# Optimization experiments

Hardware: AMD Instinct MI355X
Metric: run time of the kernel (lower is better)

The kernel has to match this reference:

```python
import jax, jax.numpy as jnp
import numpy as np

D_MODEL = 1024
N_HEAD = 16
N_KV_HEAD = 4
D_K = D_MODEL // N_HEAD          # 64
N_REP = N_HEAD // N_KV_HEAD      # 4
B, S = 2, 2048


def setup_inputs() -> dict:
    key = jax.random.key(0)
    ks = jax.random.split(key, 7)
    scale = 1.0 / np.sqrt(D_MODEL)
    return {
        "q": jax.random.normal(ks[0], (B, S, D_MODEL), jnp.float32),
        "k": jax.random.normal(ks[1], (B, S, D_MODEL), jnp.float32),
        "v": jax.random.normal(ks[2], (B, S, D_MODEL), jnp.float32),
        # weights stored [in, out] (nn.Linear applies x @ W.T; we fold the transpose)
        "W_q": jax.random.normal(ks[3], (D_MODEL, N_HEAD * D_K), jnp.float32) * scale,
        "W_k": jax.random.normal(ks[4], (D_MODEL, N_KV_HEAD * D_K), jnp.float32) * scale,
        "W_v": jax.random.normal(ks[5], (D_MODEL, N_KV_HEAD * D_K), jnp.float32) * scale,
        "W_o": jax.random.normal(ks[6], (D_MODEL, D_MODEL), jnp.float32) * scale,
    }


def reference(q, k, v, W_q, W_k, W_v, W_o):
    batch, seq_q, _ = q.shape
    seq_k = k.shape[1]
    # projections -> [b, h, s, d]
    Q = (q @ W_q).reshape(batch, seq_q, N_HEAD, D_K).transpose(0, 2, 1, 3)
    K = (k @ W_k).reshape(batch, seq_k, N_KV_HEAD, D_K).transpose(0, 2, 1, 3)
    V = (v @ W_v).reshape(batch, seq_k, N_KV_HEAD, D_K).transpose(0, 2, 1, 3)
    # repeat each KV head n_rep times consecutively (matches expand+reshape)
    K = jnp.repeat(K, N_REP, axis=1)  # [b, n_head, seq_k, d_k]
    V = jnp.repeat(V, N_REP, axis=1)
    scores = jnp.einsum('bhqd,bhkd->bhqk', Q, K) / np.sqrt(D_K).astype(jnp.float32)
    attn = jax.nn.softmax(scores, axis=-1)
    out = jnp.einsum('bhqk,bhkd->bhqd', attn, V)  # [b, h, seq_q, d_k]
    out = out.transpose(0, 2, 1, 3).reshape(batch, seq_q, D_MODEL)
    return out @ W_o
```

## Files before the change

### kernel.cpp

```cpp
#include <hip/hip_runtime.h>
#include <hip/hip_bf16.h>
#include <stdint.h>

#define DEVINL __device__ __forceinline__

typedef unsigned short u16;
typedef __bf16 bf16x8 __attribute__((ext_vector_type(8)));
typedef float f32x4 __attribute__((ext_vector_type(4)));
typedef float f32x16 __attribute__((ext_vector_type(16)));
typedef unsigned short u16x8 __attribute__((ext_vector_type(8)));
typedef unsigned int u32x4 __attribute__((ext_vector_type(4)));

constexpr int BATCH = 2, SEQ = 2048, DM = 1024, NH = 16, NKVH = 4, DK = 64;
#define QSCALE 0.18033688f

DEVINL u16 f2bf(float f) {
    unsigned u = __builtin_bit_cast(unsigned, f);
    u += 0x7fffu + ((u >> 16) & 1u);
    return (u16)(u >> 16);
}

DEVINL unsigned pkbf(float a, float b) {
    unsigned r;
    asm("v_cvt_pk_bf16_f32 %0, %1, %2" : "=v"(r) : "v"(a), "v"(b));
    return r;
}
DEVINL void swap32(unsigned& a, unsigned& b) {
    asm("v_permlane32_swap_b32 %0, %1" : "+v"(a), "+v"(b));
}
DEVINL float fexp2(float x) {
    float r;
    asm("v_exp_f32 %0, %1" : "=v"(r) : "v"(x));
    return r;
}

DEVINL void gload16(const void* g, void* l) {
    __builtin_amdgcn_global_load_lds(
        (const __attribute__((address_space(1))) unsigned int*)g,
        (__attribute__((address_space(3))) unsigned int*)l, 16, 0, 0);
}

DEVINL bf16x8 ldfrag(const u16* p) { return *reinterpret_cast<const bf16x8*>(p); }

__global__ __launch_bounds__(256) void prep_kernel(
    const float* __restrict__ q, const float* __restrict__ k, const float* __restrict__ v,
    const float* __restrict__ Wq, const float* __restrict__ Wk,
    const float* __restrict__ Wv, const float* __restrict__ Wo,
    u16* __restrict__ qb, u16* __restrict__ kb, u16* __restrict__ vb,
    u16* __restrict__ Wqt, u16* __restrict__ Wkt,
    u16* __restrict__ Wvt, u16* __restrict__ Wot) {
    __shared__ float tile[32][33];
    int bid = blockIdx.x;
    if (bid < 6144) {
        const float* in;
        u16* out;
        switch (bid >> 11) {
            case 0: in = q; out = qb; break;
            case 1: in = k; out = kb; break;
            default: in = v; out = vb; break;
        }
        int i = (bid & 2047) * 256 + threadIdx.x;
        const float4* p = reinterpret_cast<const float4*>(in) + (size_t)i * 2;
        float4 a = p[0], b = p[1];
        u16x8 o;
        o[0] = f2bf(a.x); o[1] = f2bf(a.y); o[2] = f2bf(a.z); o[3] = f2bf(a.w);
        o[4] = f2bf(b.x); o[5] = f2bf(b.y); o[6] = f2bf(b.z); o[7] = f2bf(b.w);
        reinterpret_cast<u16x8*>(out)[i] = o;
    } else {
        int tb = bid - 6144;
        int z = tb >> 10, rem = tb & 1023;
        const float* W;
        u16* Wt;
        int N;
        switch (z) {
            case 0: W = Wq; Wt = Wqt; N = 1024; break;
            case 1: W = Wk; Wt = Wkt; N = 256; break;
            case 2: W = Wv; Wt = Wvt; N = 256; break;
            default: W = Wo; Wt = Wot; N = 1024; break;
        }
        int n0 = (rem & 31) * 32;
        if (n0 >= N) return;
        int k0 = (rem >> 5) * 32;
        int tx = threadIdx.x & 31, ty = threadIdx.x >> 5;
#pragma unroll
        for (int r = 0; r < 4; ++r)
            tile[ty + 8 * r][tx] = W[(size_t)(k0 + ty + 8 * r) * N + n0 + tx];
        __syncthreads();
#pragma unroll
        for (int r = 0; r < 4; ++r)
            Wt[(size_t)(n0 + ty + 8 * r) * 1024 + k0 + tx] = f2bf(tile[tx][ty + 8 * r]);
    }
}

#define GEMM_CORE64(Apt, Bpt)                                                 \
    __shared__ __align__(16) u16 Al[2][128 * 32];                             \
    __shared__ __align__(16) u16 Bl[2][64 * 32];                              \
    const int tid = threadIdx.x;                                              \
    const int lane = tid & 63;                                                \
    const int w = tid >> 6;                                                   \
    const u16* Ab = (Apt) + (size_t)m0 * 1024;                                \
    const u16* Bb = (Bpt) + (size_t)n0 * 1024;                                \
    f32x4 acc[2][4] = {};                                                     \
    auto stage = [&](int buf, int kt) {                                       \
        const u16* Ag = Ab + kt * 32;                                         \
        const u16* Bg = Bb + kt * 32;                                         \
        _Pragma("unroll") for (int rnd = 0; rnd < 2; ++rnd) {                 \
            int L = tid * 16 + rnd * 4096;                                    \
            int row = L >> 6;                                                 \
            int cb = (L & 63) ^ (((row >> 1) & 3) << 4);                      \
            gload16(Ag + (size_t)row * 1024 + (cb >> 1), &Al[buf][L >> 1]);   \
        }                                                                     \
        {                                                                     \
            int L = tid * 16;                                                 \
            int row = L >> 6;                                                 \
            int cb = (L & 63) ^ (((row >> 1) & 3) << 4);                      \
            gload16(Bg + (size_t)row * 1024 + (cb >> 1), &Bl[buf][L >> 1]);   \
        }                                                                     \
    };                                                                        \
    stage(0, 0);                                                              \
    __syncthreads();                                                          \
    int buf = 0;                                                              \
    for (int kt = 0; kt < 32; ++kt) {                                         \
        if (kt + 1 < 32) stage(buf ^ 1, kt + 1);                              \
        bf16x8 af[2], bfr[4];                                                 \
        _Pragma("unroll") for (int mi = 0; mi < 2; ++mi) {                    \
            int row = w * 32 + mi * 16 + (lane & 15);                         \
            int cb = ((lane >> 4) * 16) ^ (((row >> 1) & 3) << 4);            \
            af[mi] = ldfrag(&Al[buf][row * 32 + (cb >> 1)]);                  \
        }                                                                     \
        _Pragma("unroll") for (int ni = 0; ni < 4; ++ni) {                    \
            int row = ni * 16 + (lane & 15);                                  \
            int cb = ((lane >> 4) * 16) ^ (((row >> 1) & 3) << 4);            \
            bfr[ni] = ldfrag(&Bl[buf][row * 32 + (cb >> 1)]);                 \
        }                                                                     \
        _Pragma("unroll") for (int mi = 0; mi < 2; ++mi)                      \
            _Pragma("unroll") for (int ni = 0; ni < 4; ++ni)                  \
                acc[mi][ni] = __builtin_amdgcn_mfma_f32_16x16x32_bf16(        \
                    af[mi], bfr[ni], acc[mi][ni], 0, 0, 0);                   \
        __syncthreads();                                                      \
        buf ^= 1;                                                             \
    }

__global__ __launch_bounds__(256) void proj_kernel(
    const u16* __restrict__ qb, const u16* __restrict__ kb, const u16* __restrict__ vb,
    const u16* __restrict__ Wqt, const u16* __restrict__ Wkt, const u16* __restrict__ Wvt,
    u16* __restrict__ Qp, u16* __restrict__ Kf, u16* __restrict__ Vf) {
    int bid = blockIdx.x;
    int tile = (bid & 7) * 96 + (bid >> 3);
    const u16 *A, *Bt;
    int m0, n0, z;
    if (tile < 512) {
        z = 0; A = qb; Bt = Wqt; m0 = (tile >> 4) * 128; n0 = (tile & 15) * 64;
    } else if (tile < 640) {
        int t = tile - 512;
        z = 1; A = kb; Bt = Wkt; m0 = (t >> 2) * 128; n0 = (t & 3) * 64;
    } else {
        int t = tile - 640;
        z = 2; A = vb; Bt = Wvt; m0 = (t >> 2) * 128; n0 = (t & 3) * 64;
    }

    GEMM_CORE64(A, Bt)

#pragma unroll
    for (int mi = 0; mi < 2; ++mi)
#pragma unroll
        for (int ni = 0; ni < 4; ++ni)
#pragma unroll
            for (int r = 0; r < 4; ++r) {
                int row = m0 + w * 32 + mi * 16 + (lane >> 4) * 4 + r;
                int col = n0 + ni * 16 + (lane & 15);
                float v = acc[mi][ni][r];
                int bb = row >> 11, s = row & 2047;
                int hh = col >> 6, dd = col & 63;
                if (z == 0) {
                    Qp[((((size_t)bb * NH + hh) * 2048 + s) << 6) + dd] = f2bf(v * QSCALE);
                } else if (z == 1) {
                    size_t base = (size_t)(bb * NKVH + hh) * 131072;
                    int s32 = s >> 5, q31s = s & 31;
                    int c = dd >> 4, hib = (dd >> 3) & 1, j = dd & 7;
                    Kf[base + (size_t)((s32 * 4 + c) * 64 + hib * 32 + q31s) * 8 + j] = f2bf(v);
                } else {
                    size_t base = (size_t)(bb * NKVH + hh) * 131072;
                    int kt = s >> 6, i = (s >> 4) & 3, hib = (s >> 3) & 1, j = s & 7;
                    int dt = dd >> 5, q31v = dd & 31;
                    Vf[base + (size_t)((((kt * 2 + dt) * 4 + i) * 64) + hib * 32 + q31v) * 8 + j] = f2bf(v);
                }
            }
}

__global__ __launch_bounds__(256) void oproj_kernel(const u16* __restrict__ Oa,
                                                    const u16* __restrict__ Wot,
                                                    float* __restrict__ out) {
    int bid = blockIdx.x;
    int tile = (bid & 7) * 64 + (bid >> 3);
    const int m0 = (tile >> 4) * 128, n0 = (tile & 15) * 64;

    GEMM_CORE64(Oa, Wot)

#pragma unroll
    for (int mi = 0; mi < 2; ++mi)
#pragma unroll
        for (int ni = 0; ni < 4; ++ni)
#pragma unroll
            for (int r = 0; r < 4; ++r) {
                int row = m0 + w * 32 + mi * 16 + (lane >> 4) * 4 + r;
                int col = n0 + ni * 16 + (lane & 15);
                out[(size_t)row * 1024 + col] = acc[mi][ni][r];
            }
}

__global__ __launch_bounds__(256) void attn_kernel(const u16* __restrict__ Qp,
                                                   const u16* __restrict__ Kf,
                                                   const u16* __restrict__ Vf,
                                                   u16* __restrict__ Oa) {
    __shared__ __align__(16) u16 Kl[4][4096];
    __shared__ __align__(16) u16 Vl[4][4096];

    const int tid = threadIdx.x;
    const int lane = tid & 63, w = tid >> 6;
    const int hi = lane >> 5, q31 = lane & 31;
    const int qt = blockIdx.x, h = blockIdx.y, b = blockIdx.z;
    const int kvh = h >> 2;
    const int qrow = qt * 128 + w * 32 + q31;

    const u16* Qb = Qp + ((size_t)((b * NH + h) * SEQ) + qrow) * 64 + hi * 8;
    bf16x8 qf0 = ldfrag(Qb), qf1 = ldfrag(Qb + 16);
    bf16x8 qf2 = ldfrag(Qb + 32), qf3 = ldfrag(Qb + 48);

    const u16* KbG = Kf + (size_t)(b * NKVH + kvh) * 131072;
    const u16* VbG = Vf + (size_t)(b * NKVH + kvh) * 131072;

    auto stageT = [&](int slot, int tile) {
        const u16* Kg = KbG + (size_t)tile * 4096 + lane * 8;
        const u16* Vg = VbG + (size_t)tile * 4096 + lane * 8;
        gload16(Kg + w * 512, &Kl[slot][w * 512]);
        gload16(Kg + (w + 4) * 512, &Kl[slot][(w + 4) * 512]);
        gload16(Vg + w * 512, &Vl[slot][w * 512]);
        gload16(Vg + (w + 4) * 512, &Vl[slot][(w + 4) * 512]);
    };

    f32x16 od0 = {}, od1 = {};
    float lsum = 0.f;
    f32x16 sA0 = {}, sA1 = {}, sB0 = {}, sB1 = {};
    bf16x8 kA[8], kB[8], vf[8];

    stageT(0, 0);
    stageT(1, 1);
    stageT(2, 2);
    asm volatile("s_waitcnt vmcnt(0)" ::: "memory");
    __builtin_amdgcn_s_barrier();

#pragma unroll
    for (int r = 0; r < 8; ++r) kA[r] = ldfrag(&Kl[0][r * 512 + lane * 8]);
    sA0 = __builtin_amdgcn_mfma_f32_32x32x16_bf16(kA[0], qf0, sA0, 0, 0, 0);
    sA0 = __builtin_amdgcn_mfma_f32_32x32x16_bf16(kA[1], qf1, sA0, 0, 0, 0);
    sA0 = __builtin_amdgcn_mfma_f32_32x32x16_bf16(kA[2], qf2, sA0, 0, 0, 0);
    sA0 = __builtin_amdgcn_mfma_f32_32x32x16_bf16(kA[3], qf3, sA0, 0, 0, 0);
    sA1 = __builtin_amdgcn_mfma_f32_32x32x16_bf16(kA[4], qf0, sA1, 0, 0, 0);
    sA1 = __builtin_amdgcn_mfma_f32_32x32x16_bf16(kA[5], qf1, sA1, 0, 0, 0);
    sA1 = __builtin_amdgcn_mfma_f32_32x32x16_bf16(kA[6], qf2, sA1, 0, 0, 0);
    sA1 = __builtin_amdgcn_mfma_f32_32x32x16_bf16(kA[7], qf3, sA1, 0, 0, 0);
#pragma unroll
    for (int r = 0; r < 8; ++r) kB[r] = ldfrag(&Kl[1][r * 512 + lane * 8]);
#pragma unroll
    for (int r = 0; r < 8; ++r) vf[r] = ldfrag(&Vl[0][r * 512 + lane * 8]);

#define PACKP(sv, s, outf)                                    \
        {                                                     \
            unsigned x0 = pkbf(sv[8 * s + 0], sv[8 * s + 1]); \
            unsigned x1 = pkbf(sv[8 * s + 2], sv[8 * s + 3]); \
            unsigned y0 = pkbf(sv[8 * s + 4], sv[8 * s + 5]); \
            unsigned y1 = pkbf(sv[8 * s + 6], sv[8 * s + 7]); \
            swap32(x0, y0);                                   \
            swap32(x1, y1);                                   \
            u32x4 tt2 = {x0, x1, y0, y1};                     \
            outf = __builtin_bit_cast(bf16x8, tt2);           \
        }

#define BODY(SC0, SC1, SN0, SN1, KQK, KLD, T)                                 \
    {                                                                         \
        __builtin_amdgcn_s_setprio(1);                                        \
        SN0 = {};                                                             \
        SN1 = {};                                                             \
        SN0 = __builtin_amdgcn_mfma_f32_32x32x16_bf16(KQK[0], qf0, SN0, 0, 0, 0); \
        SN0 = __builtin_amdgcn_mfma_f32_32x32x16_bf16(KQK[1], qf1, SN0, 0, 0, 0); \
        SN0 = __builtin_amdgcn_mfma_f32_32x32x16_bf16(KQK[2], qf2, SN0, 0, 0, 0); \
        SN0 = __builtin_amdgcn_mfma_f32_32x32x16_bf16(KQK[3], qf3, SN0, 0, 0, 0); \
        SN1 = __builtin_amdgcn_mfma_f32_32x32x16_bf16(KQK[4], qf0, SN1, 0, 0, 0); \
        SN1 = __builtin_amdgcn_mfma_f32_32x32x16_bf16(KQK[5], qf1, SN1, 0, 0, 0); \
        SN1 = __builtin_amdgcn_mfma_f32_32x32x16_bf16(KQK[6], qf2, SN1, 0, 0, 0); \
        SN1 = __builtin_amdgcn_mfma_f32_32x32x16_bf16(KQK[7], qf3, SN1, 0, 0, 0); \
        __builtin_amdgcn_s_setprio(0);                                        \
        stageT(((T) + 3) & 3, ((T) + 3) & 31);                                \
        {                                                                     \
            const u16* Ksl = &Kl[((T) + 2) & 3][lane * 8];                    \
            _Pragma("unroll") for (int r = 0; r < 8; ++r)                     \
                KLD[r] = ldfrag(Ksl + r * 512);                               \
        }                                                                     \
        _Pragma("unroll") for (int r = 0; r < 16; ++r) {                      \
            SC0[r] = fexp2(SC0[r]);                                           \
            SC1[r] = fexp2(SC1[r]);                                           \
        }                                                                     \
        {                                                                     \
            f32x16 ts = SC0 + SC1;                                            \
            float u0 = (ts[0] + ts[1]) + (ts[2] + ts[3]);                     \
            float u1 = (ts[4] + ts[5]) + (ts[6] + ts[7]);                     \
            float u2 = (ts[8] + ts[9]) + (ts[10] + ts[11]);                   \
            float u3 = (ts[12] + ts[13]) + (ts[14] + ts[15]);                 \
            lsum += (u0 + u1) + (u2 + u3);                                    \
        }                                                                     \
        bf16x8 pa0, pa1, pa2, pa3;                                            \
        PACKP(SC0, 0, pa0)                                                    \
        PACKP(SC0, 1, pa1)                                                    \
        PACKP(SC1, 0, pa2)                                                    \
        PACKP(SC1, 1, pa3)                                                    \
        __builtin_amdgcn_s_setprio(1);                                        \
        od0 = __builtin_amdgcn_mfma_f32_32x32x16_bf16(vf[0], pa0, od0, 0, 0, 0); \
        od0 = __builtin_amdgcn_mfma_f32_32x32x16_bf16(vf[1], pa1, od0, 0, 0, 0); \
        od0 = __builtin_amdgcn_mfma_f32_32x32x16_bf16(vf[2], pa2, od0, 0, 0, 0); \
        od0 = __builtin_amdgcn_mfma_f32_32x32x16_bf16(vf[3], pa3, od0, 0, 0, 0); \
        od1 = __builtin_amdgcn_mfma_f32_32x32x16_bf16(vf[4], pa0, od1, 0, 0, 0); \
        od1 = __builtin_amdgcn_mfma_f32_32x32x16_bf16(vf[5], pa1, od1, 0, 0, 0); \
        od1 = __builtin_amdgcn_mfma_f32_32x32x16_bf16(vf[6], pa2, od1, 0, 0, 0); \
        od1 = __builtin_amdgcn_mfma_f32_32x32x16_bf16(vf[7], pa3, od1, 0, 0, 0); \
        __builtin_amdgcn_s_setprio(0);                                        \
        {                                                                     \
            const u16* Vsl = &Vl[((T) + 1) & 3][lane * 8];                    \
            _Pragma("unroll") for (int r = 0; r < 8; ++r)                     \
                vf[r] = ldfrag(Vsl + r * 512);                                \
        }                                                                     \
        asm volatile("s_waitcnt vmcnt(0)" ::: "memory");                      \
        __builtin_amdgcn_s_barrier();                                         \
    }

    for (int tt = 0; tt < 16; ++tt) {
        int t = tt * 2;
        BODY(sA0, sA1, sB0, sB1, kB, kA, t)
        BODY(sB0, sB1, sA0, sA1, kA, kB, t + 1)
    }
#undef BODY
#undef PACKP

    lsum += __shfl_xor(lsum, 32);

    float inv = 1.0f / lsum;
    u16* Ob = Oa + ((size_t)(b * SEQ) + qrow) * DM + h * 64;
#pragma unroll
    for (int i = 0; i < 8; ++i) {
        int r = 2 * i;
        int d = (r & 3) + 8 * (r >> 2) + 4 * hi;
        *(unsigned*)(Ob + d) = pkbf(od0[r] * inv, od0[r + 1] * inv);
        *(unsigned*)(Ob + 32 + d) = pkbf(od1[r] * inv, od1[r + 1] * inv);
    }
}

extern "C" void kernel_launch(void* const* d_in, const int* in_sizes, int n_in,
                              void* d_out, int out_size, void* d_ws, size_t ws_size,
                              hipStream_t stream) {
    const float* q  = (const float*)d_in[0];
    const float* k  = (const float*)d_in[1];
    const float* v  = (const float*)d_in[2];
    const float* Wq = (const float*)d_in[3];
    const float* Wk = (const float*)d_in[4];
    const float* Wv = (const float*)d_in[5];
    const float* Wo = (const float*)d_in[6];
    float* out = (float*)d_out;

    char* ws = (char*)d_ws;
    u16* qb  = (u16*)(ws + (size_t)0);
    u16* kb  = (u16*)(ws + ((size_t)8 << 20));
    u16* vb  = (u16*)(ws + ((size_t)16 << 20));
    u16* Wqt = (u16*)(ws + ((size_t)24 << 20));
    u16* Wkt = (u16*)(ws + ((size_t)26 << 20));
    u16* Wvt = (u16*)(ws + ((size_t)27 << 20));
    u16* Wot = (u16*)(ws + ((size_t)28 << 20));
    u16* Qp  = (u16*)(ws + ((size_t)30 << 20));
    u16* Kf  = (u16*)(ws + ((size_t)38 << 20));
    u16* Vf  = (u16*)(ws + ((size_t)40 << 20));
    u16* Oa  = (u16*)(ws + ((size_t)42 << 20));

    prep_kernel<<<10240, 256, 0, stream>>>(q, k, v, Wq, Wk, Wv, Wo,
                                           qb, kb, vb, Wqt, Wkt, Wvt, Wot);

    proj_kernel<<<768, 256, 0, stream>>>(qb, kb, vb, Wqt, Wkt, Wvt,
                                         Qp, Kf, Vf);

    attn_kernel<<<dim3(16, 16, 2), 256, 0, stream>>>(Qp, Kf, Vf, Oa);

    oproj_kernel<<<512, 256, 0, stream>>>(Oa, Wot, out);
}
```

Measured before the change: 113.9 us.

## Fuse fp32-to-bf16 activation conversion into projection GEMM; compute softmax sum via MFMA

The prep kernel no longer converts q/k/v to bf16. The projection kernel now loads fp32 activations straight into registers, packs them to bf16 and writes them into swizzled LDS, prefetching one k-tile ahead. This removes a full read and write of the bf16 activation copies. In attention, the softmax row sum is now accumulated with an MFMA against a ones vector instead of scalar adds and a shuffle, and score accumulators start from a zero constant. The MFMA sum uses the bf16-rounded probabilities, which adds some MFMA work and slightly changes numerics.

```diff
diff --git a/kernel.cpp b/kernel.cpp
--- a/kernel.cpp
+++ b/kernel.cpp
@@ -43,53 +43,33 @@
 DEVINL bf16x8 ldfrag(const u16* p) { return *reinterpret_cast<const bf16x8*>(p); }
 
 __global__ __launch_bounds__(256) void prep_kernel(
-    const float* __restrict__ q, const float* __restrict__ k, const float* __restrict__ v,
     const float* __restrict__ Wq, const float* __restrict__ Wk,
     const float* __restrict__ Wv, const float* __restrict__ Wo,
-    u16* __restrict__ qb, u16* __restrict__ kb, u16* __restrict__ vb,
     u16* __restrict__ Wqt, u16* __restrict__ Wkt,
     u16* __restrict__ Wvt, u16* __restrict__ Wot) {
     __shared__ float tile[32][33];
     int bid = blockIdx.x;
-    if (bid < 6144) {
-        const float* in;
-        u16* out;
-        switch (bid >> 11) {
-            case 0: in = q; out = qb; break;
-            case 1: in = k; out = kb; break;
-            default: in = v; out = vb; break;
-        }
-        int i = (bid & 2047) * 256 + threadIdx.x;
-        const float4* p = reinterpret_cast<const float4*>(in) + (size_t)i * 2;
-        float4 a = p[0], b = p[1];
-        u16x8 o;
-        o[0] = f2bf(a.x); o[1] = f2bf(a.y); o[2] = f2bf(a.z); o[3] = f2bf(a.w);
-        o[4] = f2bf(b.x); o[5] = f2bf(b.y); o[6] = f2bf(b.z); o[7] = f2bf(b.w);
-        reinterpret_cast<u16x8*>(out)[i] = o;
-    } else {
-        int tb = bid - 6144;
-        int z = tb >> 10, rem = tb & 1023;
-        const float* W;
-        u16* Wt;
-        int N;
-        switch (z) {
-            case 0: W = Wq; Wt = Wqt; N = 1024; break;
-            case 1: W = Wk; Wt = Wkt; N = 256; break;
-            case 2: W = Wv; Wt = Wvt; N = 256; break;
-            default: W = Wo; Wt = Wot; N = 1024; break;
-        }
-        int n0 = (rem & 31) * 32;
-        if (n0 >= N) return;
-        int k0 = (rem >> 5) * 32;
-        int tx = threadIdx.x & 31, ty = threadIdx.x >> 5;
-#pragma unroll
-        for (int r = 0; r < 4; ++r)
-            tile[ty + 8 * r][tx] = W[(size_t)(k0 + ty + 8 * r) * N + n0 + tx];
-        __syncthreads();
-#pragma unroll
-        for (int r = 0; r < 4; ++r)
-            Wt[(size_t)(n0 + ty + 8 * r) * 1024 + k0 + tx] = f2bf(tile[tx][ty + 8 * r]);
-    }
+    int z = bid >> 10, rem = bid & 1023;
+    const float* W;
+    u16* Wt;
+    int N;
+    switch (z) {
+        case 0: W = Wq; Wt = Wqt; N = 1024; break;
+        case 1: W = Wk; Wt = Wkt; N = 256; break;
+        case 2: W = Wv; Wt = Wvt; N = 256; break;
+        default: W = Wo; Wt = Wot; N = 1024; break;
+    }
+    int n0 = (rem & 31) * 32;
+    if (n0 >= N) return;
+    int k0 = (rem >> 5) * 32;
+    int tx = threadIdx.x & 31, ty = threadIdx.x >> 5;
+#pragma unroll
+    for (int r = 0; r < 4; ++r)
+        tile[ty + 8 * r][tx] = W[(size_t)(k0 + ty + 8 * r) * N + n0 + tx];
+    __syncthreads();
+#pragma unroll
+    for (int r = 0; r < 4; ++r)
+        Wt[(size_t)(n0 + ty + 8 * r) * 1024 + k0 + tx] = f2bf(tile[tx][ty + 8 * r]);
 }
 
 #define GEMM_CORE64(Apt, Bpt)                                                 \
@@ -142,24 +122,94 @@
     }
 
 __global__ __launch_bounds__(256) void proj_kernel(
-    const u16* __restrict__ qb, const u16* __restrict__ kb, const u16* __restrict__ vb,
+    const float* __restrict__ q32, const float* __restrict__ k32, const float* __restrict__ v32,
     const u16* __restrict__ Wqt, const u16* __restrict__ Wkt, const u16* __restrict__ Wvt,
     u16* __restrict__ Qp, u16* __restrict__ Kf, u16* __restrict__ Vf) {
     int bid = blockIdx.x;
     int tile = (bid & 7) * 96 + (bid >> 3);
-    const u16 *A, *Bt;
+    const float* A32;
+    const u16* Bt;
     int m0, n0, z;
     if (tile < 512) {
-        z = 0; A = qb; Bt = Wqt; m0 = (tile >> 4) * 128; n0 = (tile & 15) * 64;
+        z = 0; A32 = q32; Bt = Wqt; m0 = (tile >> 4) * 128; n0 = (tile & 15) * 64;
     } else if (tile < 640) {
         int t = tile - 512;
-        z = 1; A = kb; Bt = Wkt; m0 = (t >> 2) * 128; n0 = (t & 3) * 64;
+        z = 1; A32 = k32; Bt = Wkt; m0 = (t >> 2) * 128; n0 = (t & 3) * 64;
     } else {
         int t = tile - 640;
-        z = 2; A = vb; Bt = Wvt; m0 = (t >> 2) * 128; n0 = (t & 3) * 64;
-    }
-
-    GEMM_CORE64(A, Bt)
+        z = 2; A32 = v32; Bt = Wvt; m0 = (t >> 2) * 128; n0 = (t & 3) * 64;
+    }
+
+    __shared__ __align__(16) u16 Al[2][128 * 32];
+    __shared__ __align__(16) u16 Bl[2][64 * 32];
+    const int tid = threadIdx.x;
+    const int lane = tid & 63;
+    const int w = tid >> 6;
+    const float* Ab32 = A32 + (size_t)m0 * 1024;
+    const u16* Bb = Bt + (size_t)n0 * 1024;
+    f32x4 acc[2][4] = {};
+
+    const int L0 = tid * 16, row0 = L0 >> 6, colb0 = L0 & 63;
+    const int L1 = L0 + 4096, row1 = L1 >> 6, colb1 = L1 & 63;
+    const int dst0 = row0 * 64 + (colb0 ^ (((row0 >> 1) & 3) << 4));
+    const int dst1 = row1 * 64 + (colb1 ^ (((row1 >> 1) & 3) << 4));
+    const int cbB = colb0 ^ (((row0 >> 1) & 3) << 4);
+    const float* srcA0 = Ab32 + (size_t)row0 * 1024 + (colb0 >> 1);
+    const float* srcA1 = Ab32 + (size_t)row1 * 1024 + (colb1 >> 1);
+    const u16* srcB = Bb + (size_t)row0 * 1024 + (cbB >> 1);
+
+    auto packwr = [&](int buf, float4 a, float4 b, int dst) {
+        u32x4 pk;
+        pk[0] = pkbf(a.x, a.y); pk[1] = pkbf(a.z, a.w);
+        pk[2] = pkbf(b.x, b.y); pk[3] = pkbf(b.z, b.w);
+        *(u32x4*)((char*)&Al[buf][0] + dst) = pk;
+    };
+
+    {
+        float4 a0 = *(const float4*)srcA0, b0 = *(const float4*)(srcA0 + 4);
+        float4 a1 = *(const float4*)srcA1, b1 = *(const float4*)(srcA1 + 4);
+        gload16(srcB, &Bl[0][L0 >> 1]);
+        packwr(0, a0, b0, dst0);
+        packwr(0, a1, b1, dst1);
+    }
+    __syncthreads();
+
+    int buf = 0;
+    for (int kt = 0; kt < 32; ++kt) {
+        float4 a0, b0, a1, b1;
+        if (kt + 1 < 32) {
+            const float* s0 = srcA0 + (kt + 1) * 32;
+            const float* s1 = srcA1 + (kt + 1) * 32;
+            a0 = *(const float4*)s0; b0 = *(const float4*)(s0 + 4);
+            a1 = *(const float4*)s1; b1 = *(const float4*)(s1 + 4);
+            gload16(srcB + (kt + 1) * 32, &Bl[buf ^ 1][L0 >> 1]);
+        }
+        bf16x8 af[2], bfr[4];
+#pragma unroll
+        for (int mi = 0; mi < 2; ++mi) {
+            int row = w * 32 + mi * 16 + (lane & 15);
+            int cb = ((lane >> 4) * 16) ^ (((row >> 1) & 3) << 4);
+            af[mi] = ldfrag(&Al[buf][row * 32 + (cb >> 1)]);
+        }
+#pragma unroll
+        for (int ni = 0; ni < 4; ++ni) {
+            int row = ni * 16 + (lane & 15);
+            int cb = ((lane >> 4) * 16) ^ (((row >> 1) & 3) << 4);
+            bfr[ni] = ldfrag(&Bl[buf][row * 32 + (cb >> 1)]);
+        }
+#pragma unroll
+        for (int mi = 0; mi < 2; ++mi)
+#pragma unroll
+            for (int ni = 0; ni < 4; ++ni)
+                acc[mi][ni] = __builtin_amdgcn_mfma_f32_16x16x32_bf16(
+                    af[mi], bfr[ni], acc[mi][ni], 0, 0, 0);
+        if (kt + 1 < 32) {
+            packwr(buf ^ 1, a0, b0, dst0);
+            packwr(buf ^ 1, a1, b1, dst1);
+        }
+        __syncthreads();
+        buf ^= 1;
+    }
 
 #pragma unroll
     for (int mi = 0; mi < 2; ++mi)
@@ -239,9 +289,14 @@
         gload16(Vg + (w + 4) * 512, &Vl[slot][(w + 4) * 512]);
     };
 
-    f32x16 od0 = {}, od1 = {};
-    float lsum = 0.f;
-    f32x16 sA0 = {}, sA1 = {}, sB0 = {}, sB1 = {};
+    u16x8 ov;
+#pragma unroll
+    for (int j = 0; j < 8; ++j) ov[j] = 0x3F80;
+    const bf16x8 ones = __builtin_bit_cast(bf16x8, ov);
+    const f32x16 ZF = {};
+
+    f32x16 od0 = {}, od1 = {}, lacc = {};
+    f32x16 sA0, sA1, sB0, sB1;
     bf16x8 kA[8], kB[8], vf[8];
 
     stageT(0, 0);
@@ -252,11 +307,11 @@
 
 #pragma unroll
     for (int r = 0; r < 8; ++r) kA[r] = ldfrag(&Kl[0][r * 512 + lane * 8]);
-    sA0 = __builtin_amdgcn_mfma_f32_32x32x16_bf16(kA[0], qf0, sA0, 0, 0, 0);
+    sA0 = __builtin_amdgcn_mfma_f32_32x32x16_bf16(kA[0], qf0, ZF, 0, 0, 0);
     sA0 = __builtin_amdgcn_mfma_f32_32x32x16_bf16(kA[1], qf1, sA0, 0, 0, 0);
     sA0 = __builtin_amdgcn_mfma_f32_32x32x16_bf16(kA[2], qf2, sA0, 0, 0, 0);
     sA0 = __builtin_amdgcn_mfma_f32_32x32x16_bf16(kA[3], qf3, sA0, 0, 0, 0);
-    sA1 = __builtin_amdgcn_mfma_f32_32x32x16_bf16(kA[4], qf0, sA1, 0, 0, 0);
+    sA1 = __builtin_amdgcn_mfma_f32_32x32x16_bf16(kA[4], qf0, ZF, 0, 0, 0);
     sA1 = __builtin_amdgcn_mfma_f32_32x32x16_bf16(kA[5], qf1, sA1, 0, 0, 0);
     sA1 = __builtin_amdgcn_mfma_f32_32x32x16_bf16(kA[6], qf2, sA1, 0, 0, 0);
     sA1 = __builtin_amdgcn_mfma_f32_32x32x16_bf16(kA[7], qf3, sA1, 0, 0, 0);
@@ -280,13 +335,11 @@
 #define BODY(SC0, SC1, SN0, SN1, KQK, KLD, T)                                 \
     {                                                                         \
         __builtin_amdgcn_s_setprio(1);                                        \
-        SN0 = {};                                                             \
-        SN1 = {};                                                             \
-        SN0 = __builtin_amdgcn_mfma_f32_32x32x16_bf16(KQK[0], qf0, SN0, 0, 0, 0); \
+        SN0 = __builtin_amdgcn_mfma_f32_32x32x16_bf16(KQK[0], qf0, ZF, 0, 0, 0); \
         SN0 = __builtin_amdgcn_mfma_f32_32x32x16_bf16(KQK[1], qf1, SN0, 0, 0, 0); \
         SN0 = __builtin_amdgcn_mfma_f32_32x32x16_bf16(KQK[2], qf2, SN0, 0, 0, 0); \
         SN0 = __builtin_amdgcn_mfma_f32_32x32x16_bf16(KQK[3], qf3, SN0, 0, 0, 0); \
-        SN1 = __builtin_amdgcn_mfma_f32_32x32x16_bf16(KQK[4], qf0, SN1, 0, 0, 0); \
+        SN1 = __builtin_amdgcn_mfma_f32_32x32x16_bf16(KQK[4], qf0, ZF, 0, 0, 0); \
         SN1 = __builtin_amdgcn_mfma_f32_32x32x16_bf16(KQK[5], qf1, SN1, 0, 0, 0); \
         SN1 = __builtin_amdgcn_mfma_f32_32x32x16_bf16(KQK[6], qf2, SN1, 0, 0, 0); \
         SN1 = __builtin_amdgcn_mfma_f32_32x32x16_bf16(KQK[7], qf3, SN1, 0, 0, 0); \
@@ -301,20 +354,16 @@
             SC0[r] = fexp2(SC0[r]);                                           \
             SC1[r] = fexp2(SC1[r]);                                           \
         }                                                                     \
-        {                                                                     \
-            f32x16 ts = SC0 + SC1;                                            \
-            float u0 = (ts[0] + ts[1]) + (ts[2] + ts[3]);                     \
-            float u1 = (ts[4] + ts[5]) + (ts[6] + ts[7]);                     \
-            float u2 = (ts[8] + ts[9]) + (ts[10] + ts[11]);                   \
-            float u3 = (ts[12] + ts[13]) + (ts[14] + ts[15]);                 \
-            lsum += (u0 + u1) + (u2 + u3);                                    \
-        }                                                                     \
         bf16x8 pa0, pa1, pa2, pa3;                                            \
         PACKP(SC0, 0, pa0)                                                    \
         PACKP(SC0, 1, pa1)                                                    \
         PACKP(SC1, 0, pa2)                                                    \
         PACKP(SC1, 1, pa3)                                                    \
         __builtin_amdgcn_s_setprio(1);                                        \
+        lacc = __builtin_amdgcn_mfma_f32_32x32x16_bf16(ones, pa0, lacc, 0, 0, 0); \
+        lacc = __builtin_amdgcn_mfma_f32_32x32x16_bf16(ones, pa1, lacc, 0, 0, 0); \
+        lacc = __builtin_amdgcn_mfma_f32_32x32x16_bf16(ones, pa2, lacc, 0, 0, 0); \
+        lacc = __builtin_amdgcn_mfma_f32_32x32x16_bf16(ones, pa3, lacc, 0, 0, 0); \
         od0 = __builtin_amdgcn_mfma_f32_32x32x16_bf16(vf[0], pa0, od0, 0, 0, 0); \
         od0 = __builtin_amdgcn_mfma_f32_32x32x16_bf16(vf[1], pa1, od0, 0, 0, 0); \
         od0 = __builtin_amdgcn_mfma_f32_32x32x16_bf16(vf[2], pa2, od0, 0, 0, 0); \
@@ -341,9 +390,7 @@
 #undef BODY
 #undef PACKP
 
-    lsum += __shfl_xor(lsum, 32);
-
-    float inv = 1.0f / lsum;
+    float inv = 1.0f / lacc[0];
     u16* Ob = Oa + ((size_t)(b * SEQ) + qrow) * DM + h * 64;
 #pragma unroll
     for (int i = 0; i < 8; ++i) {
@@ -367,23 +414,18 @@
     float* out = (float*)d_out;
 
     char* ws = (char*)d_ws;
-    u16* qb  = (u16*)(ws + (size_t)0);
-    u16* kb  = (u16*)(ws + ((size_t)8 << 20));
-    u16* vb  = (u16*)(ws + ((size_t)16 << 20));
-    u16* Wqt = (u16*)(ws + ((size_t)24 << 20));
-    u16* Wkt = (u16*)(ws + ((size_t)26 << 20));
-    u16* Wvt = (u16*)(ws + ((size_t)27 << 20));
-    u16* Wot = (u16*)(ws + ((size_t)28 << 20));
-    u16* Qp  = (u16*)(ws + ((size_t)30 << 20));
-    u16* Kf  = (u16*)(ws + ((size_t)38 << 20));
-    u16* Vf  = (u16*)(ws + ((size_t)40 << 20));
-    u16* Oa  = (u16*)(ws + ((size_t)42 << 20));
-
-    prep_kernel<<<10240, 256, 0, stream>>>(q, k, v, Wq, Wk, Wv, Wo,
-                                           qb, kb, vb, Wqt, Wkt, Wvt, Wot);
-
-    proj_kernel<<<768, 256, 0, stream>>>(qb, kb, vb, Wqt, Wkt, Wvt,
-                                         Qp, Kf, Vf);
+    u16* Wqt = (u16*)(ws + (size_t)0);
+    u16* Wkt = (u16*)(ws + ((size_t)2 << 20));
+    u16* Wvt = (u16*)(ws + ((size_t)3 << 20));
+    u16* Wot = (u16*)(ws + ((size_t)4 << 20));
+    u16* Qp  = (u16*)(ws + ((size_t)6 << 20));
+    u16* Kf  = (u16*)(ws + ((size_t)14 << 20));
+    u16* Vf  = (u16*)(ws + ((size_t)16 << 20));
+    u16* Oa  = (u16*)(ws + ((size_t)18 << 20));
+
+    prep_kernel<<<4096, 256, 0, stream>>>(Wq, Wk, Wv, Wo, Wqt, Wkt, Wvt, Wot);
+
+    proj_kernel<<<768, 256, 0, stream>>>(q, k, v, Wqt, Wkt, Wvt, Qp, Kf, Vf);
 
     attn_kernel<<<dim3(16, 16, 2), 256, 0, stream>>>(Qp, Kf, Vf, Oa);
 
```

Result: slower. 127.3 us (+11.8%).
